# Kernel tuning notes

Measured on AMD Instinct MI355X. Metric: run time of the kernel, lower is better.

Reference implementation:

```python
import jax, jax.numpy as jnp
import numpy as np

B, T, V, E, H = 16, 32, 1003, 100, 2048


def setup_inputs() -> dict:
    key = jax.random.key(0)
    ks = jax.random.split(key, 16)
    s = 0.02
    n = lambda k, shape: (jax.random.normal(k, shape, jnp.float32) * s)
    tokens = jax.random.randint(ks[0], (B, T), 0, V, dtype=jnp.int32)
    return {
        "tokens": tokens,
        "emb": n(ks[1], (V, E)),
        "W1": n(ks[2], (E, 4 * H)), "U1": n(ks[3], (H, 4 * H)), "b1": jnp.zeros((4 * H,), jnp.float32),
        "W2": n(ks[4], (H, 4 * H)), "U2": n(ks[5], (H, 4 * H)), "b2": jnp.zeros((4 * H,), jnp.float32),
        "W3": n(ks[6], (H, 4 * H)), "U3": n(ks[7], (H, 4 * H)), "b3": jnp.zeros((4 * H,), jnp.float32),
        "Wd1": n(ks[8], (H, H)), "bd1": jnp.zeros((H,), jnp.float32),
        "Wd2": n(ks[9], (H, V)), "bd2": jnp.zeros((V,), jnp.float32),
    }


def masked_lstm(x, mask, W, U, b):
    """Keras-semantics masked LSTM. x: [B,T,D], mask: [B,T] bool.
    Masked steps carry h,c through unchanged (cuDNN-incompatible path).
    Returns (all_h: [B,T,H], last_h: [B,H])."""
    Hd = U.shape[0]
    Bd = x.shape[0]
    # precompute input projections for all timesteps at once: [T,B,4H]
    xz = jnp.einsum('btd,dh->tbh', x, W) + b
    m_t = jnp.swapaxes(mask, 0, 1)  # [T,B]

    def step(carry, inp):
        h, c = carry
        zx, mt = inp
        z = zx + h @ U  # [B,4H]
        i, f, g, o = jnp.split(z, 4, axis=-1)
        i = jax.nn.sigmoid(i)
        f = jax.nn.sigmoid(f)
        g = jnp.tanh(g)
        o = jax.nn.sigmoid(o)
        c_new = f * c + i * g
        h_new = o * jnp.tanh(c_new)
        m = mt[:, None]
        h_new = jnp.where(m, h_new, h)
        c_new = jnp.where(m, c_new, c)
        return (h_new, c_new), h_new

    init = (jnp.zeros((Bd, Hd), x.dtype), jnp.zeros((Bd, Hd), x.dtype))
    (h_last, _), hs = jax.lax.scan(step, init, (xz, m_t))
    return jnp.swapaxes(hs, 0, 1), h_last


def reference(tokens, emb, W1, U1, b1, W2, U2, b2, W3, U3, b3, Wd1, bd1, Wd2, bd2):
    mask = tokens != 0  # mask_zero=True semantics
    x = emb[tokens]  # [B,T,E]
    x, _ = masked_lstm(x, mask, W1, U1, b1)
    x, _ = masked_lstm(x, mask, W2, U2, b2)
    _, h = masked_lstm(x, mask, W3, U3, b3)  # return_sequences=False -> last (carried) state
    y = h @ Wd1 + bd1  # Dense, linear activation
    logits = y @ Wd2 + bd2
    return jax.nn.softmax(logits, axis=-1)
```

## Files before the change

### kernel.cpp

```cpp
#include <hip/hip_runtime.h>
#include <hip/hip_bf16.h>
#include <cstddef>

#define BB 16
#define TT 32
#define VV 1003
#define EE 100
#define HH 2048
#define G4 8192

typedef __attribute__((ext_vector_type(4))) float f32x4;
typedef unsigned char u8;

#define SA 64.0f
#define SB 128.0f
#define DESCALE 1.220703125e-4f

__device__ __forceinline__ unsigned pk_lo(unsigned old, float a, float b) {
  return (unsigned)__builtin_amdgcn_cvt_pk_fp8_f32(a, b, (int)old, false);
}
__device__ __forceinline__ unsigned pk_hi(unsigned old, float a, float b) {
  return (unsigned)__builtin_amdgcn_cvt_pk_fp8_f32(a, b, (int)old, true);
}
__device__ __forceinline__ u8 cvt1fp8(float a) {
  return (u8)(__builtin_amdgcn_cvt_pk_fp8_f32(a, 0.f, 0, false) & 0xff);
}
__device__ __forceinline__ long mklong(unsigned lo, unsigned hi) {
  return (long)(((unsigned long long)hi << 32) | lo);
}

__global__ __launch_bounds__(256) void embed_frag(
    const int* __restrict__ tokens, const float* __restrict__ emb,
    u8* __restrict__ xf) {
  int i = blockIdx.x * 256 + threadIdx.x;
  if (i >= TT * BB * 128) return;
  int e = i & 127, b = (i >> 7) & 15, t = i >> 11;
  float v = 0.f;
  if (e < EE) v = emb[(size_t)tokens[b * TT + t] * EE + e] * SA;
  int kt = e >> 5, kk = e & 31;
  int lane = (kk >> 3) * 16 + b, j = kk & 7;
  xf[(size_t)t * 2048 + (size_t)(kt >> 1) * 1024 + lane * 16 + (kt & 1) * 8 + j] =
      cvt1fp8(v);
}

__global__ __launch_bounds__(256) void split_fp8(
    const float* __restrict__ src, u8* __restrict__ dst,
    int Kreal, int nkt2) {
  __shared__ float ld[64][257];
  int tid = threadIdx.x;
  int pair = blockIdx.x, ct0 = blockIdx.y * 16;
  int r0 = pair * 64;

#pragma unroll
  for (int i = 0; i < 16; i++) {
    int elem = i * 1024 + tid * 4;
    int row = elem >> 8, c = elem & 255;
    int g = c >> 6, rel = c & 63;
    int r = r0 + row;
    float4 v = make_float4(0.f, 0.f, 0.f, 0.f);
    if (r < Kreal)
      v = *(const float4*)&src[(size_t)r * G4 + (size_t)g * HH + ct0 * 4 + rel];
    ld[row][c] = v.x; ld[row][c + 1] = v.y;
    ld[row][c + 2] = v.z; ld[row][c + 3] = v.w;
  }
  __syncthreads();

  int L = tid & 63;
  int cl = L & 15, g = cl >> 2, hq = cl & 3;
  int row0 = (L >> 4) * 8;
#pragma unroll
  for (int pass = 0; pass < 4; pass++) {
    int ctr = (tid >> 6) + pass * 4;
    int col = g * 64 + ctr * 4 + hq;
    unsigned lo0 = 0, hi0 = 0, lo1 = 0, hi1 = 0;
    lo0 = pk_lo(lo0, ld[row0 + 0][col] * SB, ld[row0 + 1][col] * SB);
    lo0 = pk_hi(lo0, ld[row0 + 2][col] * SB, ld[row0 + 3][col] * SB);
    hi0 = pk_lo(hi0, ld[row0 + 4][col] * SB, ld[row0 + 5][col] * SB);
    hi0 = pk_hi(hi0, ld[row0 + 6][col] * SB, ld[row0 + 7][col] * SB);
    lo1 = pk_lo(lo1, ld[32 + row0 + 0][col] * SB, ld[32 + row0 + 1][col] * SB);
    lo1 = pk_hi(lo1, ld[32 + row0 + 2][col] * SB, ld[32 + row0 + 3][col] * SB);
    hi1 = pk_lo(hi1, ld[32 + row0 + 4][col] * SB, ld[32 + row0 + 5][col] * SB);
    hi1 = pk_hi(hi1, ld[32 + row0 + 6][col] * SB, ld[32 + row0 + 7][col] * SB);
    *(uint4*)&dst[((size_t)(ct0 + ctr) * nkt2 + pair) * 1024 + L * 16] =
        make_uint4(lo0, hi0, lo1, hi1);
  }
}

__global__ __launch_bounds__(512) void gemm_mfma(
    const u8* __restrict__ af, int t_stride, int nkt2,
    const u8* __restrict__ wfrag, const float* __restrict__ bias,
    float* __restrict__ xz) {
  __shared__ __align__(16) u8 Bs[3][8][1024];
  int tid = threadIdx.x;
  int w = tid >> 6, L = tid & 63;
  int ct0 = blockIdx.x * 8;
  int t_a = blockIdx.y * 4 + (w & 3);
  int nt0 = (w >> 2) * 4;

  f32x4 acc[4];
#pragma unroll
  for (int i = 0; i < 4; i++) acc[i] = (f32x4){0.f, 0.f, 0.f, 0.f};
  const u8* Ah = af + (size_t)t_a * t_stride + L * 16;

  int s_nt = tid >> 6, boff = (tid & 63) * 16;

  {
    uint4 t0 = *(const uint4*)&wfrag[((size_t)(ct0 + s_nt) * nkt2 + 0) * 1024 + boff];
    *(uint4*)&Bs[0][s_nt][boff] = t0;
    if (nkt2 > 1) {
      uint4 t1 = *(const uint4*)&wfrag[((size_t)(ct0 + s_nt) * nkt2 + 1) * 1024 + boff];
      *(uint4*)&Bs[1][s_nt][boff] = t1;
    }
  }
  __syncthreads();

  for (int s = 0; s < nkt2; s++) {
    uint4 nx;
    bool pf = (s + 2 < nkt2);
    if (pf)
      nx = *(const uint4*)&wfrag[((size_t)(ct0 + s_nt) * nkt2 + s + 2) * 1024 + boff];
    int buf = s % 3;
    uint4 a = *(const uint4*)(Ah + (size_t)s * 1024);
    long a0 = mklong(a.x, a.y), a1 = mklong(a.z, a.w);
#pragma unroll
    for (int i = 0; i < 4; i++) {
      uint4 bb = *(const uint4*)&Bs[buf][nt0 + i][L * 16];
      acc[i] = __builtin_amdgcn_mfma_f32_16x16x32_fp8_fp8(a0, mklong(bb.x, bb.y), acc[i], 0, 0, 0);
      acc[i] = __builtin_amdgcn_mfma_f32_16x16x32_fp8_fp8(a1, mklong(bb.z, bb.w), acc[i], 0, 0, 0);
    }
    if (pf) *(uint4*)&Bs[(s + 2) % 3][s_nt][boff] = nx;
    __syncthreads();
  }

  int nq = L >> 4, hl = L & 15;
#pragma unroll
  for (int i = 0; i < 4; i++) {
    int ctg = ct0 + nt0 + i;
    int gcol = (hl >> 2) * HH + ctg * 4 + (hl & 3);
    float bv = bias[gcol];
#pragma unroll
    for (int r = 0; r < 4; r++) {
      int b = nq * 4 + r;
      xz[((size_t)t_a * 16 + b) * G4 + ctg * 16 + hl] = acc[i][r] * DESCALE + bv;
    }
  }
}

__global__ __launch_bounds__(512, 4) void lstm_step(
    const u8* __restrict__ Ufrag,
    const float* __restrict__ xzt,
    const u8* __restrict__ hf_in,
    u8* __restrict__ hf_out,
    const float* __restrict__ hT_in,
    float* __restrict__ hT_out,
    float* __restrict__ c,
    const int* __restrict__ tokens, int t) {
  __shared__ float red[8][16][16];
  __shared__ float zs[16][16];
  int tid = threadIdx.x, w = tid >> 6, L = tid & 63;
  int ct = blockIdx.x;

  float xzv = 0.f;
  if (tid < 256) xzv = xzt[(size_t)(tid >> 4) * G4 + ct * 16 + (tid & 15)];
  float c_old = 0.f, h_old = 0.f;
  int tok = 1;
  if (tid < 64) {
    int b = tid >> 2, hq = tid & 3;
    int hu = ct * 4 + hq;
    c_old = c[(size_t)b * HH + hu];
    h_old = hT_in[(size_t)hu * BB + b];
    tok = tokens[b * TT + t];
  }

  f32x4 acc = {0.f, 0.f, 0.f, 0.f};
  const u8* Ub = Ufrag + ((size_t)ct * 32 + w * 4) * 1024 + L * 16;
  const u8* Hb = hf_in + (size_t)(w * 4) * 1024 + L * 16;

#pragma unroll
  for (int i = 0; i < 4; i++) {
    uint4 u = *(const uint4*)(Ub + i * 1024);
    uint4 h = *(const uint4*)(Hb + i * 1024);
    acc = __builtin_amdgcn_mfma_f32_16x16x32_fp8_fp8(mklong(h.x, h.y), mklong(u.x, u.y), acc, 0, 0, 0);
    acc = __builtin_amdgcn_mfma_f32_16x16x32_fp8_fp8(mklong(h.z, h.w), mklong(u.z, u.w), acc, 0, 0, 0);
  }
#pragma unroll
  for (int r = 0; r < 4; r++) red[w][(L >> 4) * 4 + r][L & 15] = acc[r];
  __syncthreads();

  if (tid < 256) {
    int b = tid >> 4, cl = tid & 15;
    float s = 0.f;
#pragma unroll
    for (int q = 0; q < 8; q++) s += red[q][b][cl];
    zs[b][cl] = s * DESCALE + xzv;
  }
  __syncthreads();

  if (tid < 64) {
    int b = tid >> 2, hq = tid & 3;
    int hu = ct * 4 + hq;
    float z0 = zs[b][0 + hq];
    float z1 = zs[b][4 + hq];
    float z2 = zs[b][8 + hq];
    float z3 = zs[b][12 + hq];
    float ig = 1.f / (1.f + expf(-z0));
    float fg = 1.f / (1.f + expf(-z1));
    float gt = tanhf(z2);
    float og = 1.f / (1.f + expf(-z3));
    float cn = fg * c_old + ig * gt;
    float hn = og * tanhf(cn);
    if (tok == 0) {
      cn = c_old;
      hn = h_old;
    }
    c[(size_t)b * HH + hu] = cn;
    hT_out[(size_t)hu * BB + b] = hn;
    int kt2 = hu >> 5, kk = hu & 31;
    int lane2 = (kk >> 3) * 16 + b, jj = kk & 7;
    hf_out[(size_t)(kt2 >> 1) * 1024 + lane2 * 16 + (kt2 & 1) * 8 + jj] =
        cvt1fp8(hn * SA);
  }
}

__global__ __launch_bounds__(256) void head_partial(
    const float* __restrict__ XT, const float* __restrict__ W,
    float* __restrict__ partial, int N) {
  __shared__ float xs[2048];
  int tid = threadIdx.x;
  int k0 = blockIdx.y * 128;
  const float* src = XT + (size_t)k0 * 16;
  for (int i = tid; i < 2048; i += 256) xs[i] = src[i];
  __syncthreads();
  int kg = tid >> 6, lane = tid & 63;
  int col = blockIdx.x * 64 + lane;
  if (col >= N) return;
  float acc[16];
#pragma unroll
  for (int b = 0; b < 16; b++) acc[b] = 0.f;
  const float* Wp = W + (size_t)(k0 + kg * 32) * N + col;
  const float* xp = xs + kg * 32 * 16;
  for (int kk = 0; kk < 32; kk++) {
    float wv = Wp[(size_t)kk * N];
#pragma unroll
    for (int b = 0; b < 16; b++) acc[b] = fmaf(xp[kk * 16 + b], wv, acc[b]);
  }
  int chunk = blockIdx.y * 4 + kg;
#pragma unroll
  for (int b = 0; b < 16; b++)
    partial[((size_t)chunk * 16 + b) * N + col] = acc[b];
}

__global__ __launch_bounds__(256) void head_reduce(
    const float* __restrict__ partial, const float* __restrict__ bias,
    float* __restrict__ out, int N, int sc, int sb) {
  int i = blockIdx.x * 256 + threadIdx.x;
  if (i >= 16 * N) return;
  int b = i / N, col = i - b * N;
  float s = bias[col];
#pragma unroll 8
  for (int ch = 0; ch < 64; ch++) s += partial[((size_t)ch * 16 + b) * N + col];
  out[(size_t)col * sc + (size_t)b * sb] = s;
}

__global__ __launch_bounds__(256) void softmax_rows(
    const float* __restrict__ logits, float* __restrict__ out, int N) {
  __shared__ float buf[1024];
  __shared__ float wred[4];
  __shared__ float rmax, rsum;
  int b = blockIdx.x, tid = threadIdx.x;
  float m = -1e30f;
  for (int v = tid; v < N; v += 256) {
    float x = logits[(size_t)b * N + v];
    buf[v] = x;
    m = fmaxf(m, x);
  }
  for (int o = 32; o > 0; o >>= 1) m = fmaxf(m, __shfl_down(m, o, 64));
  if ((tid & 63) == 0) wred[tid >> 6] = m;
  __syncthreads();
  if (tid == 0) rmax = fmaxf(fmaxf(wred[0], wred[1]), fmaxf(wred[2], wred[3]));
  __syncthreads();
  float s = 0.f;
  for (int v = tid; v < N; v += 256) {
    float e = expf(buf[v] - rmax);
    buf[v] = e;
    s += e;
  }
  for (int o = 32; o > 0; o >>= 1) s += __shfl_down(s, o, 64);
  if ((tid & 63) == 0) wred[tid >> 6] = s;
  __syncthreads();
  if (tid == 0) rsum = wred[0] + wred[1] + wred[2] + wred[3];
  __syncthreads();
  float inv = 1.f / rsum;
  for (int v = tid; v < N; v += 256) out[(size_t)b * N + v] = buf[v] * inv;
}

extern "C" void kernel_launch(void* const* d_in, const int* in_sizes, int n_in,
                              void* d_out, int out_size, void* d_ws, size_t ws_size,
                              hipStream_t stream) {
  const int*   tokens = (const int*)d_in[0];
  const float* emb  = (const float*)d_in[1];
  const float* W1   = (const float*)d_in[2];
  const float* U1   = (const float*)d_in[3];
  const float* b1   = (const float*)d_in[4];
  const float* W2   = (const float*)d_in[5];
  const float* U2   = (const float*)d_in[6];
  const float* b2   = (const float*)d_in[7];
  const float* W3   = (const float*)d_in[8];
  const float* U3   = (const float*)d_in[9];
  const float* b3   = (const float*)d_in[10];
  const float* Wd1  = (const float*)d_in[11];
  const float* bd1  = (const float*)d_in[12];
  const float* Wd2  = (const float*)d_in[13];
  const float* bd2  = (const float*)d_in[14];
  float* out = (float*)d_out;

  char* base = (char*)d_ws;
  size_t off = 0;
  auto carve = [&](size_t bytes) -> char* {
    char* p = base + off;
    off += (bytes + 255) & ~(size_t)255;
    return p;
  };
  float* xz      = (float*)carve((size_t)TT * BB * G4 * 4);
  u8*    allhf0  = (u8*)carve(33ull * 32768);
  u8*    allhf1  = (u8*)carve(33ull * 32768);
  u8*    allhf2  = (u8*)carve(33ull * 32768);
  u8*    xfrag   = (u8*)carve((size_t)TT * 2048);
  u8*    wfrag   = (u8*)carve(512ull * 64 * 512);
  u8*    ufrag   = (u8*)carve(512ull * 64 * 512);
  float* hT0     = (float*)carve(2 * HH * BB * 4);
  float* cbuf    = hT0 + HH * BB;
  float* hT1     = (float*)carve(HH * BB * 4);
  float* yT      = (float*)carve(HH * BB * 4);
  float* logits  = (float*)carve(BB * 1024 * 4);
  float* partial = (float*)carve(64ull * 16 * HH * 4);

  u8* allhf[3] = {allhf0, allhf1, allhf2};
  const float* Us[3] = {U1, U2, U3};
  const float* Ws[3] = {W1, W2, W3};
  const float* bs[3] = {b1, b2, b3};
  float* hping[2] = {hT0, hT1};

  embed_frag<<<dim3(256), 256, 0, stream>>>(tokens, emb, xfrag);

  for (int layer = 0; layer < 3; layer++) {
    const u8* af;
    int t_stride, nkt2W, KrealW;
    if (layer == 0) {
      af = xfrag; t_stride = 2048; nkt2W = 2; KrealW = EE;
    } else {
      af = allhf[layer - 1] + 32768;
      t_stride = 32768; nkt2W = 32; KrealW = HH;
    }
    split_fp8<<<dim3(nkt2W, 32), 256, 0, stream>>>(Ws[layer], wfrag, KrealW, nkt2W);
    gemm_mfma<<<dim3(64, 8), 512, 0, stream>>>(
        af, t_stride, nkt2W, wfrag, bs[layer], xz);
    split_fp8<<<dim3(32, 32), 256, 0, stream>>>(Us[layer], ufrag, HH, 32);

    (void)hipMemsetAsync(allhf[layer], 0, 32768, stream);
    (void)hipMemsetAsync(hT0, 0, 2 * HH * BB * 4, stream);
    for (int t = 0; t < TT; t++) {
      lstm_step<<<dim3(512), 512, 0, stream>>>(
          ufrag, xz + (size_t)t * BB * G4,
          allhf[layer] + (size_t)t * 32768, allhf[layer] + (size_t)(t + 1) * 32768,
          hping[t & 1], hping[(t + 1) & 1], cbuf, tokens, t);
    }
  }

  head_partial<<<dim3(HH / 64, 16), 256, 0, stream>>>(hT0, Wd1, partial, HH);
  head_reduce<<<dim3((16 * HH + 255) / 256), 256, 0, stream>>>(partial, bd1, yT, HH, 16, 1);
  head_partial<<<dim3((VV + 63) / 64, 16), 256, 0, stream>>>(yT, Wd2, partial, VV);
  head_reduce<<<dim3((16 * VV + 255) / 256), 256, 0, stream>>>(partial, bd2, logits, VV, 1, VV);
  softmax_rows<<<dim3(BB), 256, 0, stream>>>(logits, out, VV);
}
```

Baseline: 669.3 us.

## Fuse W/U fp8 splits, fold memsets into GEMM, widen LSTM step to 1024 threads

Merges the W and U fp8 fragment conversion into a single launch, and moves the per-layer zeroing of the initial hidden fragments and transposed h buffers into the first row of gemm_mfma blocks, removing two memset calls and one kernel launch per layer. The recurrent step kernel now uses 16 waves per block, each handling two K tiles instead of four, with a larger shared reduction. This aims to cut launch overhead and shorten per-step latency on the serial critical path. The cost is a larger cross-wave reduction and heavier register and occupancy pressure per block.

```diff
diff --git a/kernel.cpp b/kernel.cpp
--- a/kernel.cpp
+++ b/kernel.cpp
@@ -43,14 +43,11 @@
       cvt1fp8(v);
 }
 
-__global__ __launch_bounds__(256) void split_fp8(
+__device__ __forceinline__ void split_body(
     const float* __restrict__ src, u8* __restrict__ dst,
-    int Kreal, int nkt2) {
+    int Kreal, int nkt2, int pair, int ct0, int tid) {
   __shared__ float ld[64][257];
-  int tid = threadIdx.x;
-  int pair = blockIdx.x, ct0 = blockIdx.y * 16;
   int r0 = pair * 64;
-
 #pragma unroll
   for (int i = 0; i < 16; i++) {
     int elem = i * 1024 + tid * 4;
@@ -86,16 +83,35 @@
   }
 }
 
+__global__ __launch_bounds__(256) void split_wu(
+    const float* __restrict__ srcW, u8* __restrict__ dstW, int KrealW, int nkt2W,
+    const float* __restrict__ srcU, u8* __restrict__ dstU) {
+  int tid = threadIdx.x;
+  int bx = blockIdx.x, ct0 = blockIdx.y * 16;
+  if (bx < nkt2W)
+    split_body(srcW, dstW, KrealW, nkt2W, bx, ct0, tid);
+  else
+    split_body(srcU, dstU, HH, 32, bx - nkt2W, ct0, tid);
+}
+
 __global__ __launch_bounds__(512) void gemm_mfma(
     const u8* __restrict__ af, int t_stride, int nkt2,
     const u8* __restrict__ wfrag, const float* __restrict__ bias,
-    float* __restrict__ xz) {
+    float* __restrict__ xz,
+    unsigned* __restrict__ hzero,
+    unsigned* __restrict__ hcz) {
   __shared__ __align__(16) u8 Bs[3][8][1024];
   int tid = threadIdx.x;
   int w = tid >> 6, L = tid & 63;
   int ct0 = blockIdx.x * 8;
   int t_a = blockIdx.y * 4 + (w & 3);
   int nt0 = (w >> 2) * 4;
+
+  if (blockIdx.y == 0) {
+    if (tid < 128) hzero[blockIdx.x * 128 + tid] = 0u;
+    hcz[blockIdx.x * 1024 + tid] = 0u;
+    hcz[blockIdx.x * 1024 + 512 + tid] = 0u;
+  }
 
   f32x4 acc[4];
 #pragma unroll
@@ -146,7 +162,7 @@
   }
 }
 
-__global__ __launch_bounds__(512, 4) void lstm_step(
+__global__ __launch_bounds__(1024, 8) void lstm_step(
     const u8* __restrict__ Ufrag,
     const float* __restrict__ xzt,
     const u8* __restrict__ hf_in,
@@ -155,7 +171,7 @@
     float* __restrict__ hT_out,
     float* __restrict__ c,
     const int* __restrict__ tokens, int t) {
-  __shared__ float red[8][16][16];
+  __shared__ float red[16][16][16];
   __shared__ float zs[16][16];
   int tid = threadIdx.x, w = tid >> 6, L = tid & 63;
   int ct = blockIdx.x;
@@ -173,11 +189,11 @@
   }
 
   f32x4 acc = {0.f, 0.f, 0.f, 0.f};
-  const u8* Ub = Ufrag + ((size_t)ct * 32 + w * 4) * 1024 + L * 16;
-  const u8* Hb = hf_in + (size_t)(w * 4) * 1024 + L * 16;
-
-#pragma unroll
-  for (int i = 0; i < 4; i++) {
+  const u8* Ub = Ufrag + ((size_t)ct * 32 + w * 2) * 1024 + L * 16;
+  const u8* Hb = hf_in + (size_t)(w * 2) * 1024 + L * 16;
+
+#pragma unroll
+  for (int i = 0; i < 2; i++) {
     uint4 u = *(const uint4*)(Ub + i * 1024);
     uint4 h = *(const uint4*)(Hb + i * 1024);
     acc = __builtin_amdgcn_mfma_f32_16x16x32_fp8_fp8(mklong(h.x, h.y), mklong(u.x, u.y), acc, 0, 0, 0);
@@ -191,7 +207,7 @@
     int b = tid >> 4, cl = tid & 15;
     float s = 0.f;
 #pragma unroll
-    for (int q = 0; q < 8; q++) s += red[q][b][cl];
+    for (int q = 0; q < 16; q++) s += red[q][b][cl];
     zs[b][cl] = s * DESCALE + xzv;
   }
   __syncthreads();
@@ -352,15 +368,13 @@
       af = allhf[layer - 1] + 32768;
       t_stride = 32768; nkt2W = 32; KrealW = HH;
     }
-    split_fp8<<<dim3(nkt2W, 32), 256, 0, stream>>>(Ws[layer], wfrag, KrealW, nkt2W);
+    split_wu<<<dim3(nkt2W + 32, 32), 256, 0, stream>>>(
+        Ws[layer], wfrag, KrealW, nkt2W, Us[layer], ufrag);
     gemm_mfma<<<dim3(64, 8), 512, 0, stream>>>(
-        af, t_stride, nkt2W, wfrag, bs[layer], xz);
-    split_fp8<<<dim3(32, 32), 256, 0, stream>>>(Us[layer], ufrag, HH, 32);
-
-    (void)hipMemsetAsync(allhf[layer], 0, 32768, stream);
-    (void)hipMemsetAsync(hT0, 0, 2 * HH * BB * 4, stream);
+        af, t_stride, nkt2W, wfrag, bs[layer], xz,
+        (unsigned*)allhf[layer], (unsigned*)hT0);
     for (int t = 0; t < TT; t++) {
-      lstm_step<<<dim3(512), 512, 0, stream>>>(
+      lstm_step<<<dim3(512), 1024, 0, stream>>>(
           ufrag, xz + (size_t)t * BB * G4,
           allhf[layer] + (size_t)t * 32768, allhf[layer] + (size_t)(t + 1) * 32768,
           hping[t & 1], hping[(t + 1) & 1], cbuf, tokens, t);
```

Result: faster. 645.1 us (-3.6%).
